# Kernel optimization log

Hardware: AMD Instinct MI355X
Metric: run time of the kernel (lower is better)

## Reference

```python
import jax, jax.numpy as jnp
import numpy as np

RADIUS, HEAD, SLOT, DIM = 16.0, 8, 112, 512

def _l2norm(x, axis):
    n = jnp.linalg.norm(x, axis=axis, keepdims=True)
    return x / jnp.maximum(n, 1e-12)

def _layernorm(x, g, b, eps=1e-5):
    mu = jnp.mean(x, axis=-1, keepdims=True)
    var = jnp.mean((x - mu) ** 2, axis=-1, keepdims=True)
    return (x - mu) / jnp.sqrt(var + eps) * g + b

def setup_inputs() -> dict:
    key = jax.random.key(0)
    ks = jax.random.split(key, 12)
    B, S = 32, 512
    return {
        "query": jax.random.normal(ks[0], (B, S, DIM), jnp.float32),
        "value": jax.random.normal(ks[1], (B, S, DIM), jnp.float32),
        "key_mem": jax.random.normal(ks[2], (HEAD * SLOT, DIM // HEAD), jnp.float32) * 0.5,
        "value_mem": jax.random.normal(ks[3], (SLOT, DIM), jnp.float32) * 0.5,
        "Wq": jax.random.normal(ks[4], (DIM, DIM), jnp.float32) * 0.02,
        "bq": jnp.zeros((DIM,), jnp.float32),
        "Wv": jax.random.normal(ks[5], (DIM, DIM), jnp.float32) * 0.02,
        "bv": jnp.zeros((DIM,), jnp.float32),
        "Wl": jax.random.normal(ks[6], (DIM, DIM * HEAD), jnp.float32) * 0.02,
        "bl": jnp.zeros((DIM,), jnp.float32),
        "g1": jnp.ones((DIM,), jnp.float32), "b1": jnp.zeros((DIM,), jnp.float32),
        "g2": jnp.ones((DIM,), jnp.float32), "b2": jnp.zeros((DIM,), jnp.float32),
        "g3": jnp.ones((DIM,), jnp.float32), "b3": jnp.zeros((DIM,), jnp.float32),
    }

def reference(query, value, key_mem, value_mem, Wq, bq, Wv, bv, Wl, bl,
              g1, b1, g2, b2, g3, b3):
    B, S, C = query.shape
    mq = query.reshape(B * S, C)                                   # (BS, 512)
    # --- key addressing (read path) ---
    key_norm = _l2norm(key_mem.reshape(HEAD, SLOT, -1), axis=2)    # (h, s, 64)
    eq = _l2norm((mq @ Wq.T + bq).reshape(B * S, HEAD, -1), axis=2)
    key_sim = jnp.einsum('bhd,hsd->bhs', eq, key_norm)             # (BS, h, s)
    key_add = jax.nn.softmax(RADIUS * key_sim, axis=2)
    m_head = jnp.einsum('bhs,sd->bhd', key_add,
                        jax.lax.stop_gradient(value_mem))          # (BS, h, 512)
    vir = _layernorm(m_head.reshape(B * S, HEAD * DIM) @ Wl.T + bl, g2, b2)
    te_fusion = _layernorm(query + vir.reshape(B, S, DIM), g1, b1)  # dropout = eval identity
    # --- value addressing (write/train path) ---
    mv = value.reshape(B * S, DIM)
    ev = jax.lax.stop_gradient(mv) @ Wv.T + bv
    value_norm = _l2norm(value_mem, axis=1)                        # (s, 512)
    value_sim = _l2norm(ev, axis=1) @ value_norm.T                 # (BS, s)
    value_add = jax.nn.softmax(RADIUS * value_sim, axis=1)
    aud = value_add @ value_mem                                    # (BS, 512)
    contrastive = 0.5 * jnp.abs(jnp.eye(SLOT, dtype=value_norm.dtype)
                                - value_norm @ value_norm.T).sum()[None]
    mvd = jax.lax.stop_gradient(mv)
    cos = (aud * mvd).sum(1) / jnp.maximum(
        jnp.linalg.norm(aud, axis=1) * jnp.linalg.norm(mvd, axis=1), 1e-8)
    recon = jnp.abs(1.0 - cos).reshape(B, S).sum(1)                # (B,)
    aud = _layernorm(aud, g3, b3)
    tr_fusion = _layernorm(query + aud.reshape(B, S, DIM), g1, b1)
    return (te_fusion, tr_fusion, recon, contrastive)
```

## Files before the change

### kernel.cpp

```cpp
#include <hip/hip_runtime.h>
#include <math.h>

#define DIMC   512
#define HEADS  8
#define SLOTS  112
#define HD     64
#define NROWS  16384
#define RADIUSF 16.0f

typedef short short8 __attribute__((ext_vector_type(8)));
typedef unsigned short ushort8 __attribute__((ext_vector_type(8)));
typedef float f32x4  __attribute__((ext_vector_type(4)));

__device__ __forceinline__ unsigned short f2bf(float f)
{
    unsigned u = __float_as_uint(f);
    unsigned r = (u + 0x7FFFu + ((u >> 16) & 1u)) >> 16;
    return (unsigned short)r;
}
__device__ __forceinline__ float bf2f(unsigned short h)
{
    return __uint_as_float((unsigned)h << 16);
}

__device__ __forceinline__ void gl16(const void* g, void* lds_wave_base)
{
    __builtin_amdgcn_global_load_lds(
        (const __attribute__((address_space(1))) unsigned int*)g,
        (__attribute__((address_space(3))) unsigned int*)lds_wave_base,
        16, 0, 0);
}

#define DPP_ADD(x, ctrl, rmask)                                               \
    (x) += __int_as_float(__builtin_amdgcn_update_dpp(                        \
               0, __float_as_int(x), (ctrl), (rmask), 0xf, true))

__device__ __forceinline__ float wsum64(float x)
{
    DPP_ADD(x, 0x111, 0xf);
    DPP_ADD(x, 0x112, 0xf);
    DPP_ADD(x, 0x114, 0xf);
    DPP_ADD(x, 0x118, 0xf);
    DPP_ADD(x, 0x142, 0xa);
    DPP_ADD(x, 0x143, 0xc);
    return __int_as_float(__builtin_amdgcn_readlane(__float_as_int(x), 63));
}

__device__ __forceinline__ void wsum64_4(float& a, float& b, float& c, float& d)
{
    DPP_ADD(a, 0x111, 0xf); DPP_ADD(b, 0x111, 0xf); DPP_ADD(c, 0x111, 0xf); DPP_ADD(d, 0x111, 0xf);
    DPP_ADD(a, 0x112, 0xf); DPP_ADD(b, 0x112, 0xf); DPP_ADD(c, 0x112, 0xf); DPP_ADD(d, 0x112, 0xf);
    DPP_ADD(a, 0x114, 0xf); DPP_ADD(b, 0x114, 0xf); DPP_ADD(c, 0x114, 0xf); DPP_ADD(d, 0x114, 0xf);
    DPP_ADD(a, 0x118, 0xf); DPP_ADD(b, 0x118, 0xf); DPP_ADD(c, 0x118, 0xf); DPP_ADD(d, 0x118, 0xf);
    DPP_ADD(a, 0x142, 0xa); DPP_ADD(b, 0x142, 0xa); DPP_ADD(c, 0x142, 0xa); DPP_ADD(d, 0x142, 0xa);
    DPP_ADD(a, 0x143, 0xc); DPP_ADD(b, 0x143, 0xc); DPP_ADD(c, 0x143, 0xc); DPP_ADD(d, 0x143, 0xc);
    a = __int_as_float(__builtin_amdgcn_readlane(__float_as_int(a), 63));
    b = __int_as_float(__builtin_amdgcn_readlane(__float_as_int(b), 63));
    c = __int_as_float(__builtin_amdgcn_readlane(__float_as_int(c), 63));
    d = __int_as_float(__builtin_amdgcn_readlane(__float_as_int(d), 63));
}

__global__ __launch_bounds__(256)
void gemm_bf16(const short* __restrict__ A, int lda,
               const short* __restrict__ B, int ldb,
               float* __restrict__ C, unsigned short* __restrict__ Cb,
               int ldc, int K, const float* __restrict__ bias, int Nvalid,
               int aZ, int bZ, int cZ)
{
    __shared__ short As[128 * 32];
    __shared__ short Bs[128 * 32];
    A += (size_t)blockIdx.z * aZ;
    B += (size_t)blockIdx.z * bZ;
    const size_t czoff = (size_t)blockIdx.z * cZ;
    const int tid  = threadIdx.x;
    const int wave = tid >> 6;
    const int lane = tid & 63;
    const int m0 = blockIdx.y * 128;
    const int n0 = blockIdx.x * 128;
    const int wm = (wave >> 1) * 64;
    const int wn = (wave & 1) * 64;

    const int srow = tid >> 2;
    const int schk = (tid & 3) * 8;

    const int fr = lane & 15;
    const int fq = (lane >> 4) * 8;

    f32x4 acc[4][4] = {};

    const short* Ag = A + (size_t)(m0 + srow) * lda + schk;
    const short* Bg = B + (size_t)(n0 + srow) * ldb + schk;

    short* asL = As + wave * 512;
    short* asU = As + 2048 + wave * 512;
    short* bsL = Bs + wave * 512;
    short* bsU = Bs + 2048 + wave * 512;

    for (int k0 = 0; k0 < K; k0 += 32) {
        gl16(Ag, asL);
        gl16(Ag + (size_t)64 * lda, asU);
        gl16(Bg, bsL);
        gl16(Bg + (size_t)64 * ldb, bsU);
        Ag += 32; Bg += 32;
        __syncthreads();
        short8 af[4], bf[4];
        #pragma unroll
        for (int i = 0; i < 4; ++i)
            af[i] = *(const short8*)&As[(wm + i * 16 + fr) * 32 + fq];
        #pragma unroll
        for (int j = 0; j < 4; ++j)
            bf[j] = *(const short8*)&Bs[(wn + j * 16 + fr) * 32 + fq];
        #pragma unroll
        for (int i = 0; i < 4; ++i)
            #pragma unroll
            for (int j = 0; j < 4; ++j)
                acc[i][j] = __builtin_amdgcn_mfma_f32_16x16x32_bf16(
                    af[i], bf[j], acc[i][j], 0, 0, 0);
        __syncthreads();
    }

    const int cr = (lane >> 4) * 4;
    const int cc = lane & 15;
    #pragma unroll
    for (int i = 0; i < 4; ++i) {
        const int grow = m0 + wm + i * 16 + cr;
        #pragma unroll
        for (int j = 0; j < 4; ++j) {
            const int gcol = n0 + wn + j * 16 + cc;
            if (gcol < Nvalid) {
                const float bb = bias ? bias[gcol] : 0.f;
                const size_t base = czoff + (size_t)grow * ldc + gcol;
                #pragma unroll
                for (int r = 0; r < 4; ++r) {
                    const float val = acc[i][j][r] + bb;
                    if (C)  C[base + (size_t)r * ldc]  = val;
                    if (Cb) Cb[base + (size_t)r * ldc] = f2bf(val);
                }
            }
        }
    }
}

__global__ __launch_bounds__(256)
void gemm_softmax(const short* __restrict__ A, int lda, int aZ,
                  const short* __restrict__ B, int ldb, int bZ,
                  int K,
                  unsigned short* __restrict__ Ob, int ldo, int oPerZ, int padN)
{
    __shared__ short As[128 * 32];
    __shared__ short Bs[128 * 32];
    __shared__ float P[128][113];
    __shared__ float hinvS[128];
    A += (size_t)blockIdx.z * aZ;
    B += (size_t)blockIdx.z * bZ;
    const int tid  = threadIdx.x;
    const int wave = tid >> 6;
    const int lane = tid & 63;
    const int m0 = blockIdx.y * 128;
    const int wm = (wave >> 1) * 64;
    const int wn = (wave & 1) * 64;
    const int srow = tid >> 2;
    const int schk = (tid & 3) * 8;
    const int fr = lane & 15;
    const int fq = (lane >> 4) * 8;

    f32x4 acc[4][4] = {};
    float ss[4] = {0.f, 0.f, 0.f, 0.f};

    const short* Ag = A + (size_t)(m0 + srow) * lda + schk;
    const short* Bg = B + (size_t)srow * ldb + schk;

    short* asL = As + wave * 512;
    short* asU = As + 2048 + wave * 512;
    short* bsL = Bs + wave * 512;
    short* bsU = Bs + 2048 + wave * 512;

    for (int k0 = 0; k0 < K; k0 += 32) {
        gl16(Ag, asL);
        gl16(Ag + (size_t)64 * lda, asU);
        gl16(Bg, bsL);
        gl16(Bg + (size_t)64 * ldb, bsU);
        Ag += 32; Bg += 32;
        __syncthreads();
        short8 af[4], bf[4];
        #pragma unroll
        for (int i = 0; i < 4; ++i)
            af[i] = *(const short8*)&As[(wm + i * 16 + fr) * 32 + fq];
        #pragma unroll
        for (int j = 0; j < 4; ++j)
            bf[j] = *(const short8*)&Bs[(wn + j * 16 + fr) * 32 + fq];
        #pragma unroll
        for (int i = 0; i < 4; ++i)
            #pragma unroll
            for (int e = 0; e < 8; ++e) {
                const float f = bf2f((unsigned short)af[i][e]);
                ss[i] += f * f;
            }
        #pragma unroll
        for (int i = 0; i < 4; ++i)
            #pragma unroll
            for (int j = 0; j < 4; ++j)
                acc[i][j] = __builtin_amdgcn_mfma_f32_16x16x32_bf16(
                    af[i], bf[j], acc[i][j], 0, 0, 0);
        __syncthreads();
    }

    #pragma unroll
    for (int i = 0; i < 4; ++i) {
        ss[i] += __shfl_xor(ss[i], 16, 64);
        ss[i] += __shfl_xor(ss[i], 32, 64);
    }
    if (lane < 16) {
        #pragma unroll
        for (int i = 0; i < 4; ++i)
            hinvS[wm + i * 16 + lane] = 1.f / fmaxf(sqrtf(ss[i]), 1e-12f);
    }

    const int cr = (lane >> 4) * 4;
    const int cc = lane & 15;
    #pragma unroll
    for (int i = 0; i < 4; ++i) {
        const int prow = wm + i * 16 + cr;
        #pragma unroll
        for (int j = 0; j < 4; ++j) {
            const int pcol = wn + j * 16 + cc;
            if (pcol < SLOTS) {
                #pragma unroll
                for (int r = 0; r < 4; ++r)
                    P[prow + r][pcol] = acc[i][j][r];
            }
        }
    }
    __syncthreads();

    const int rowt = tid >> 1;
    const int half = tid & 1;
    const int k0 = half * 56;
    const int rr = m0 + rowt;
    const float s = RADIUSF * hinvS[rowt];
    float mx = -1e30f;
    for (int k = k0; k < k0 + 56; ++k) mx = fmaxf(mx, P[rowt][k]);
    mx = fmaxf(mx, __shfl_xor(mx, 1, 64));
    float sum = 0.f;
    for (int k = k0; k < k0 + 56; ++k) {
        const float e = __expf(s * (P[rowt][k] - mx));
        P[rowt][k] = e;
        sum += e;
    }
    sum += __shfl_xor(sum, 1, 64);
    const float inv = 1.f / sum;
    unsigned short* orow = Ob + (size_t)rr * ldo + (size_t)blockIdx.z * oPerZ;
    for (int k = k0; k < k0 + 56; ++k) orow[k] = f2bf(P[rowt][k] * inv);
    if (half == 1)
        for (int k = SLOTS; k < padN; ++k) orow[k] = 0;
}

#define FUSED_LDS_DECL                                                        \
    __shared__ float U[17408];    \
    float* P = U;                                                             \
    short* As0 = (short*)U;                             \
    short* As1 = As0 + 1024;                            \
    short* Bs0 = As1 + 1024;                           \
    short* Bs1 = Bs0 + 16384;

#define FUSED_GEMM_CORE(Aptr, lda, Bptr, ldb, K)                              \
    f32x4 acc[2][4] = {};                                                     \
    {                                                                         \
        const int lrow = lane >> 2;                                           \
        const int lchk = (lane & 3) * 8;                                      \
        for (int k0 = 0; k0 < (K); k0 += 64) {                                \
            if (wave < 2)                                                     \
                gl16((Aptr) + (size_t)(m0 + wave * 16 + lrow) * (lda) + k0 + lchk, \
                     As0 + wave * 512);                                       \
            else if (wave < 4)                                                \
                gl16((Aptr) + (size_t)(m0 + (wave - 2) * 16 + lrow) * (lda) + k0 + 32 + lchk, \
                     As1 + (wave - 2) * 512);                                 \
            _Pragma("unroll")                                                 \
            for (int s = 0; s < 4; ++s) {                                     \
                const size_t brow = (size_t)(wave * 64 + s * 16 + lrow);      \
                gl16((Bptr) + brow * (ldb) + k0 + lchk,                       \
                     Bs0 + (wave * 64 + s * 16) * 32);                        \
                gl16((Bptr) + brow * (ldb) + k0 + 32 + lchk,                  \
                     Bs1 + (wave * 64 + s * 16) * 32);                        \
            }                                                                 \
            __syncthreads();                                                  \
            short8 af0[2], af1[2], bf0[4], bf1[4];                            \
            _Pragma("unroll")                                                 \
            for (int i = 0; i < 2; ++i) {                                     \
                af0[i] = *(const short8*)&As0[(i * 16 + fr) * 32 + fq];       \
                af1[i] = *(const short8*)&As1[(i * 16 + fr) * 32 + fq];       \
            }                                                                 \
            _Pragma("unroll")                                                 \
            for (int c = 0; c < 4; ++c) {                                     \
                bf0[c] = *(const short8*)&Bs0[(wave * 64 + c * 16 + fr) * 32 + fq]; \
                bf1[c] = *(const short8*)&Bs1[(wave * 64 + c * 16 + fr) * 32 + fq]; \
            }                                                                 \
            _Pragma("unroll")                                                 \
            for (int i = 0; i < 2; ++i)                                       \
                _Pragma("unroll")                                             \
                for (int c = 0; c < 4; ++c) {                                 \
                    acc[i][c] = __builtin_amdgcn_mfma_f32_16x16x32_bf16(      \
                        af0[i], bf0[c], acc[i][c], 0, 0, 0);                  \
                    acc[i][c] = __builtin_amdgcn_mfma_f32_16x16x32_bf16(      \
                        af1[i], bf1[c], acc[i][c], 0, 0, 0);                  \
                }                                                             \
            __syncthreads();                                                  \
        }                                                                     \
    }                                                                         \
    {                                                                         \
        const int cr = (lane >> 4) * 4;                                       \
        const int cc = lane & 15;                                             \
        _Pragma("unroll")                                                     \
        for (int i = 0; i < 2; ++i)                                           \
            _Pragma("unroll")                                                 \
            for (int c = 0; c < 4; ++c) {                                     \
                const int col = wave * 64 + c * 16 + cc;                      \
                _Pragma("unroll")                                             \
                for (int r = 0; r < 4; ++r)                                   \
                    P[(i * 16 + cr + r) * 516 + col] = acc[i][c][r];          \
            }                                                                 \
    }                                                                         \
    __syncthreads();

__global__ __launch_bounds__(512, 4)
void gemm_vir_te(const short* __restrict__ A, int lda,
                 const short* __restrict__ B, int ldb, int K,
                 const float* __restrict__ bias, const float* __restrict__ query,
                 const float* __restrict__ g1, const float* __restrict__ b1,
                 const float* __restrict__ g2, const float* __restrict__ b2,
                 float* __restrict__ out_te)
{
    FUSED_LDS_DECL
    const int tid = threadIdx.x;
    const int wave = tid >> 6;
    const int lane = tid & 63;
    const int m0 = blockIdx.x * 32;
    const int fr = lane & 15;
    const int fq = (lane >> 4) * 8;

    FUSED_GEMM_CORE(A, lda, B, ldb, K)

    const int c0 = lane * 8;
    float blv[8], gg2[8], bb2[8], gg1[8], bb1[8];
    *(f32x4*)&blv[0] = *(const f32x4*)(bias + c0);
    *(f32x4*)&blv[4] = *(const f32x4*)(bias + c0 + 4);
    *(f32x4*)&gg2[0] = *(const f32x4*)(g2 + c0);
    *(f32x4*)&gg2[4] = *(const f32x4*)(g2 + c0 + 4);
    *(f32x4*)&bb2[0] = *(const f32x4*)(b2 + c0);
    *(f32x4*)&bb2[4] = *(const f32x4*)(b2 + c0 + 4);
    *(f32x4*)&gg1[0] = *(const f32x4*)(g1 + c0);
    *(f32x4*)&gg1[4] = *(const f32x4*)(g1 + c0 + 4);
    *(f32x4*)&bb1[0] = *(const f32x4*)(b1 + c0);
    *(f32x4*)&bb1[4] = *(const f32x4*)(b1 + c0 + 4);

    for (int rp = 0; rp < 2; ++rp) {
        const int lr0 = wave * 4 + rp * 2;
        float x[2][8], q[2][8];
        #pragma unroll
        for (int p = 0; p < 2; ++p) {
            *(f32x4*)&x[p][0] = *(const f32x4*)&P[(lr0 + p) * 516 + c0];
            *(f32x4*)&x[p][4] = *(const f32x4*)&P[(lr0 + p) * 516 + c0 + 4];
            const size_t gbase = (size_t)(m0 + lr0 + p) * DIMC + c0;
            *(f32x4*)&q[p][0] = *(const f32x4*)(query + gbase);
            *(f32x4*)&q[p][4] = *(const f32x4*)(query + gbase + 4);
            #pragma unroll
            for (int j = 0; j < 8; ++j) x[p][j] += blv[j];
        }
        float s1[2] = {0.f, 0.f}, s2[2] = {0.f, 0.f};
        #pragma unroll
        for (int p = 0; p < 2; ++p)
            #pragma unroll
            for (int j = 0; j < 8; ++j) {
                s1[p] += x[p][j];
                s2[p] += x[p][j] * x[p][j];
            }
        wsum64_4(s1[0], s2[0], s1[1], s2[1]);

        float y[2][8];
        float t1[2] = {0.f, 0.f}, t2[2] = {0.f, 0.f};
        #pragma unroll
        for (int p = 0; p < 2; ++p) {
            const float mu = s1[p] * (1.f / DIMC);
            const float var = s2[p] * (1.f / DIMC) - mu * mu;
            const float rstd = rsqrtf(var + 1e-5f);
            #pragma unroll
            for (int j = 0; j < 8; ++j) {
                const float v = (x[p][j] - mu) * rstd * gg2[j] + bb2[j];
                y[p][j] = q[p][j] + v;
                t1[p] += y[p][j];
                t2[p] += y[p][j] * y[p][j];
            }
        }
        wsum64_4(t1[0], t2[0], t1[1], t2[1]);

        #pragma unroll
        for (int p = 0; p < 2; ++p) {
            const float mu = t1[p] * (1.f / DIMC);
            const float var = t2[p] * (1.f / DIMC) - mu * mu;
            const float rstd = rsqrtf(var + 1e-5f);
            float o[8];
            #pragma unroll
            for (int j = 0; j < 8; ++j)
                o[j] = (y[p][j] - mu) * rstd * gg1[j] + bb1[j];
            const size_t gbase = (size_t)(m0 + lr0 + p) * DIMC + c0;
            *(float4*)(out_te + gbase)     = make_float4(o[0], o[1], o[2], o[3]);
            *(float4*)(out_te + gbase + 4) = make_float4(o[4], o[5], o[6], o[7]);
        }
    }
}

__global__ __launch_bounds__(512, 4)
void gemm_aud_tr(const short* __restrict__ A, int lda,
                 const short* __restrict__ B, int ldb, int K,
                 const float* __restrict__ value, const float* __restrict__ query,
                 const float* __restrict__ g1, const float* __restrict__ b1,
                 const float* __restrict__ g3, const float* __restrict__ b3,
                 float* __restrict__ out_tr, float* __restrict__ recon)
{
    FUSED_LDS_DECL
    __shared__ float red[8];
    const int tid = threadIdx.x;
    const int wave = tid >> 6;
    const int lane = tid & 63;
    const int m0 = blockIdx.x * 32;
    const int fr = lane & 15;
    const int fq = (lane >> 4) * 8;

    FUSED_GEMM_CORE(A, lda, B, ldb, K)

    const int c0 = lane * 8;
    float gg3[8], bb3[8], gg1[8], bb1[8];
    *(f32x4*)&gg3[0] = *(const f32x4*)(g3 + c0);
    *(f32x4*)&gg3[4] = *(const f32x4*)(g3 + c0 + 4);
    *(f32x4*)&bb3[0] = *(const f32x4*)(b3 + c0);
    *(f32x4*)&bb3[4] = *(const f32x4*)(b3 + c0 + 4);
    *(f32x4*)&gg1[0] = *(const f32x4*)(g1 + c0);
    *(f32x4*)&gg1[4] = *(const f32x4*)(g1 + c0 + 4);
    *(f32x4*)&bb1[0] = *(const f32x4*)(b1 + c0);
    *(f32x4*)&bb1[4] = *(const f32x4*)(b1 + c0 + 4);

    float rloc = 0.f;
    for (int rp = 0; rp < 2; ++rp) {
        const int lr0 = wave * 4 + rp * 2;
        float a[2][8], v[2][8], q[2][8];
        #pragma unroll
        for (int p = 0; p < 2; ++p) {
            *(f32x4*)&a[p][0] = *(const f32x4*)&P[(lr0 + p) * 516 + c0];
            *(f32x4*)&a[p][4] = *(const f32x4*)&P[(lr0 + p) * 516 + c0 + 4];
            const size_t gbase = (size_t)(m0 + lr0 + p) * DIMC + c0;
            *(f32x4*)&v[p][0] = *(const f32x4*)(value + gbase);
            *(f32x4*)&v[p][4] = *(const f32x4*)(value + gbase + 4);
            *(f32x4*)&q[p][0] = *(const f32x4*)(query + gbase);
            *(f32x4*)&q[p][4] = *(const f32x4*)(query + gbase + 4);
        }
        float dot[2] = {0.f, 0.f}, na[2] = {0.f, 0.f};
        float nv[2] = {0.f, 0.f}, s1[2] = {0.f, 0.f};
        #pragma unroll
        for (int p = 0; p < 2; ++p)
            #pragma unroll
            for (int j = 0; j < 8; ++j) {
                dot[p] += a[p][j] * v[p][j];
                na[p]  += a[p][j] * a[p][j];
                nv[p]  += v[p][j] * v[p][j];
                s1[p]  += a[p][j];
            }
        wsum64_4(dot[0], na[0], nv[0], s1[0]);
        wsum64_4(dot[1], na[1], nv[1], s1[1]);

        #pragma unroll
        for (int p = 0; p < 2; ++p) {
            const float cosv = dot[p] / fmaxf(sqrtf(na[p]) * sqrtf(nv[p]), 1e-8f);
            rloc += fabsf(1.f - cosv);
        }

        float y[2][8];
        float t1[2] = {0.f, 0.f}, t2[2] = {0.f, 0.f};
        #pragma unroll
        for (int p = 0; p < 2; ++p) {
            const float mu = s1[p] * (1.f / DIMC);
            const float var = na[p] * (1.f / DIMC) - mu * mu;
            const float rstd = rsqrtf(var + 1e-5f);
            #pragma unroll
            for (int j = 0; j < 8; ++j) {
                const float w = (a[p][j] - mu) * rstd * gg3[j] + bb3[j];
                y[p][j] = q[p][j] + w;
                t1[p] += y[p][j];
                t2[p] += y[p][j] * y[p][j];
            }
        }
        wsum64_4(t1[0], t2[0], t1[1], t2[1]);

        #pragma unroll
        for (int p = 0; p < 2; ++p) {
            const float mu = t1[p] * (1.f / DIMC);
            const float var = t2[p] * (1.f / DIMC) - mu * mu;
            const float rstd = rsqrtf(var + 1e-5f);
            float o[8];
            #pragma unroll
            for (int j = 0; j < 8; ++j)
                o[j] = (y[p][j] - mu) * rstd * gg1[j] + bb1[j];
            const size_t gbase = (size_t)(m0 + lr0 + p) * DIMC + c0;
            *(float4*)(out_tr + gbase)     = make_float4(o[0], o[1], o[2], o[3]);
            *(float4*)(out_tr + gbase + 4) = make_float4(o[4], o[5], o[6], o[7]);
        }
    }

    if (lane == 0) red[wave] = rloc;
    __syncthreads();
    if (tid == 0)
        atomicAdd(&recon[m0 >> 9], red[0] + red[1] + red[2] + red[3]
                                 + red[4] + red[5] + red[6] + red[7]);
}

__device__ __forceinline__ float block_sum_256(float v, float* red)
{
    #pragma unroll
    for (int off = 32; off; off >>= 1) v += __shfl_down(v, off, 64);
    const int lane = threadIdx.x & 63, wid = threadIdx.x >> 6;
    __syncthreads();
    if (lane == 0) red[wid] = v;
    __syncthreads();
    return red[0] + red[1] + red[2] + red[3];
}

__global__ void conv_all(const float* __restrict__ q, const float* __restrict__ v,
                         const float* __restrict__ Wq, const float* __restrict__ Wv,
                         const float* __restrict__ Wl, const float* __restrict__ vm,
                         unsigned short* __restrict__ qbf, unsigned short* __restrict__ vbf,
                         unsigned short* __restrict__ wqbf, unsigned short* __restrict__ wvbf,
                         unsigned short* __restrict__ wlbf, unsigned short* __restrict__ vmbf)
{
    const int i = blockIdx.x * blockDim.x + threadIdx.x;
    const float* src;
    unsigned short* dst;
    int off;
    if (i < 2097152)      { src = q;  dst = qbf;  off = i; }
    else if (i < 4194304) { src = v;  dst = vbf;  off = i - 2097152; }
    else if (i < 4259840) { src = Wq; dst = wqbf; off = i - 4194304; }
    else if (i < 4325376) { src = Wv; dst = wvbf; off = i - 4259840; }
    else if (i < 4849664) { src = Wl; dst = wlbf; off = i - 4325376; }
    else if (i < 4864000) { src = vm; dst = vmbf; off = i - 4849664; }
    else {
        const int j = i - 4864000;
        *(ushort4*)(vmbf + 57344 + (size_t)j * 4) = make_ushort4(0, 0, 0, 0);
        return;
    }
    const float4 x = *(const float4*)(src + (size_t)off * 4);
    ushort4 o;
    o.x = f2bf(x.x); o.y = f2bf(x.y); o.z = f2bf(x.z); o.w = f2bf(x.w);
    *(ushort4*)(dst + (size_t)off * 4) = o;
}

__global__ void prep_key_norm(const float* __restrict__ km,
                              unsigned short* __restrict__ knb,
                              float* __restrict__ outrc)
{
    const int row = blockIdx.x;
    const int h = row >> 7, s = row & 127;
    const int lane = threadIdx.x;
    if (row == 0 && lane < 33) outrc[lane] = 0.f;
    const float v = (s < SLOTS) ? km[(size_t)(h * SLOTS + s) * HD + lane] : 0.f;
    const float ssum = wsum64(v * v);
    const float inv = 1.f / fmaxf(sqrtf(ssum), 1e-12f);
    knb[(size_t)row * HD + lane] = f2bf(v * inv);
}

__global__ void prep_value_norm(const float* __restrict__ vm,
                                float* __restrict__ vn,
                                unsigned short* __restrict__ vnb,
                                unsigned short* __restrict__ vmTb)
{
    const int row = blockIdx.x;
    const int tid = threadIdx.x;
    if (row >= 112) {
        const int idx = (row - 112) * 256 + tid;
        if (idx < 8192) {
            vmTb[(size_t)(idx >> 4) * 128 + 112 + (idx & 15)] = 0;
        } else {
            const int j = idx - 8192;
            vnb[(size_t)(112 + (j >> 9)) * 512 + (j & 511)] = 0;
        }
        return;
    }
    __shared__ float red[4];
    const float v0 = vm[(size_t)row * DIMC + tid];
    const float v1 = vm[(size_t)row * DIMC + 256 + tid];
    const float tot = block_sum_256(v0 * v0 + v1 * v1, red);
    const float inv = 1.f / fmaxf(sqrtf(tot), 1e-12f);
    vn[(size_t)row * DIMC + tid]        = v0 * inv;
    vn[(size_t)row * DIMC + 256 + tid]  = v1 * inv;
    vnb[(size_t)row * DIMC + tid]       = f2bf(v0 * inv);
    vnb[(size_t)row * DIMC + 256 + tid] = f2bf(v1 * inv);
    vmTb[(size_t)tid * 128 + row]         = f2bf(v0);
    vmTb[(size_t)(256 + tid) * 128 + row] = f2bf(v1);
}

__global__ void contrastive_kernel(const float* __restrict__ vn, float* __restrict__ outc)
{
    __shared__ float vni[DIMC];
    __shared__ float red[2];
    const int i = blockIdx.x, tid = threadIdx.x;
    for (int d = tid; d < DIMC; d += 128) vni[d] = vn[(size_t)i * DIMC + d];
    __syncthreads();
    float t = 0.f;
    if (tid < SLOTS) {
        const float* r = vn + (size_t)tid * DIMC;
        float dot = 0.f;
        for (int d = 0; d < DIMC; ++d) dot += vni[d] * r[d];
        const float delta = (tid == i) ? 1.f : 0.f;
        t = fabsf(delta - dot);
    }
    #pragma unroll
    for (int off = 32; off; off >>= 1) t += __shfl_down(t, off, 64);
    if ((tid & 63) == 0) red[tid >> 6] = t;
    __syncthreads();
    if (tid == 0) atomicAdd(outc, 0.5f * (red[0] + red[1]));
}

extern "C" void kernel_launch(void* const* d_in, const int* in_sizes, int n_in,
                              void* d_out, int out_size, void* d_ws, size_t ws_size,
                              hipStream_t stream)
{
    const float* query = (const float*)d_in[0];
    const float* value = (const float*)d_in[1];
    const float* keym  = (const float*)d_in[2];
    const float* vmem  = (const float*)d_in[3];
    const float* Wq    = (const float*)d_in[4];
    const float* bq    = (const float*)d_in[5];
    const float* Wv    = (const float*)d_in[6];
    const float* bv    = (const float*)d_in[7];
    const float* Wl    = (const float*)d_in[8];
    const float* bl    = (const float*)d_in[9];
    const float* g1    = (const float*)d_in[10];
    const float* b1    = (const float*)d_in[11];
    const float* g2    = (const float*)d_in[12];
    const float* b2    = (const float*)d_in[13];
    const float* g3    = (const float*)d_in[14];
    const float* b3    = (const float*)d_in[15];

    float* out    = (float*)d_out;
    float* out_te = out;
    float* out_tr = out + 8388608;
    float* out_rc = out + 16777216;

    float* ws = (float*)d_ws;
    unsigned short* w_knb  = (unsigned short*)(ws + 0);
    unsigned short* w_vmTb = (unsigned short*)(ws + 32768);
    unsigned short* w_vnb  = (unsigned short*)(ws + 65536);
    float*          w_vn   = ws + 98304;
    unsigned short* w_w2tbf= (unsigned short*)(ws + 155648);
    unsigned short* w_vmbf = (unsigned short*)(ws + 385024);
    unsigned short* w_wlbf = (unsigned short*)(ws + 417792);
    unsigned short* w_xbf  = (unsigned short*)(ws + 1466368);
    unsigned short* w_kaddc= (unsigned short*)(ws + 5660672);
    unsigned short* w_vsb  = (unsigned short*)(ws + 13000704);
    unsigned short* w_qbf  = (unsigned short*)(ws + 14049280);
    unsigned short* w_vbf  = (unsigned short*)(ws + 18243584);
    unsigned short* w_wqbf = (unsigned short*)(ws + 22437888);
    unsigned short* w_wvbf = (unsigned short*)(ws + 22568960);

    conv_all<<<19008, 256, 0, stream>>>(query, value, Wq, Wv, Wl, vmem,
                                        w_qbf, w_vbf, w_wqbf, w_wvbf,
                                        w_wlbf, w_vmbf);
    prep_key_norm<<<1024, 64, 0, stream>>>(keym, w_knb, out_rc);
    prep_value_norm<<<176, 256, 0, stream>>>(vmem, w_vn, w_vnb, w_vmTb);
    contrastive_kernel<<<112, 128, 0, stream>>>(w_vn, out_rc + 32);
    gemm_bf16<<<dim3(1, 4, 8), 256, 0, stream>>>(
        (const short*)w_wlbf, HEADS * DIMC, (const short*)w_vmbf, DIMC,
        nullptr, w_w2tbf, HEADS * SLOTS, DIMC, nullptr, SLOTS,
        DIMC, 0, SLOTS);

    gemm_bf16<<<dim3(4, 128), 256, 0, stream>>>(
        (const short*)w_qbf, DIMC, (const short*)w_wqbf, DIMC,
        nullptr, w_xbf, DIMC, DIMC, bq, DIMC, 0, 0, 0);
    gemm_softmax<<<dim3(1, 128, 8), 256, 0, stream>>>(
        (const short*)w_xbf, DIMC, HD, (const short*)w_knb, HD, 128 * HD,
        HD, w_kaddc, HEADS * SLOTS, SLOTS, SLOTS);
    gemm_vir_te<<<NROWS / 32, 512, 0, stream>>>(
        (const short*)w_kaddc, HEADS * SLOTS, (const short*)w_w2tbf, HEADS * SLOTS,
        HEADS * SLOTS, bl, query, g1, b1, g2, b2, out_te);

    gemm_bf16<<<dim3(4, 128), 256, 0, stream>>>(
        (const short*)w_vbf, DIMC, (const short*)w_wvbf, DIMC,
        nullptr, w_xbf, DIMC, DIMC, bv, DIMC, 0, 0, 0);
    gemm_softmax<<<dim3(1, 128, 1), 256, 0, stream>>>(
        (const short*)w_xbf, DIMC, 0, (const short*)w_vnb, DIMC, 0,
        DIMC, w_vsb, 128, 0, 128);
    gemm_aud_tr<<<NROWS / 32, 512, 0, stream>>>(
        (const short*)w_vsb, 128, (const short*)w_vmTb, 128, 128,
        value, query, g1, b1, g3, b3, out_tr, out_rc);
}
```

Before: 329.4 us.

## Retile vir GEMM to 64-row blocks with register-resident double layernorm epilogue

Rewrites the vir/te fused GEMM so each block computes 64 rows instead of 32. Each of the 8 waves owns a 16x256 tile, so every B tile loaded into shared memory is reused across twice as many rows. The layernorm epilogue now runs directly on the MFMA accumulators using shuffle and shared-memory row reductions, skipping the staging of the output tile through LDS. The costs are higher register and LDS use (launch bounds drop to 2 blocks per CU), half as many blocks, and uncoalesced scalar loads of query and stores of out_te in the epilogue.

```diff
diff --git a/kernel.cpp b/kernel.cpp
--- a/kernel.cpp
+++ b/kernel.cpp
@@ -253,6 +253,166 @@
     for (int k = k0; k < k0 + 56; ++k) orow[k] = f2bf(P[rowt][k] * inv);
     if (half == 1)
         for (int k = SLOTS; k < padN; ++k) orow[k] = 0;
+}
+
+__global__ __launch_bounds__(512, 2)
+void gemm_vir_te(const short* __restrict__ A, int lda,
+                 const short* __restrict__ B, int ldb, int K,
+                 const float* __restrict__ bias, const float* __restrict__ query,
+                 const float* __restrict__ g1, const float* __restrict__ b1,
+                 const float* __restrict__ g2, const float* __restrict__ b2,
+                 float* __restrict__ out_te)
+{
+    __shared__ short As0[64 * 32];
+    __shared__ short As1[64 * 32];
+    __shared__ short Bs0[512 * 32];
+    __shared__ short Bs1[512 * 32];
+    __shared__ float parm[5 * 512];
+    __shared__ float red1[128], red2[128];
+
+    const int tid  = threadIdx.x;
+    const int wave = tid >> 6;
+    const int lane = tid & 63;
+    const int m0 = blockIdx.x * 64;
+    const int s = wave >> 1;
+    const int h = wave & 1;
+    const int fr = lane & 15;
+    const int fq = (lane >> 4) * 8;
+
+    parm[tid]        = bias[tid];
+    parm[512 + tid]  = g2[tid];
+    parm[1024 + tid] = b2[tid];
+    parm[1536 + tid] = g1[tid];
+    parm[2048 + tid] = b1[tid];
+
+    f32x4 acc[16] = {};
+
+    const int lrow = lane >> 2;
+    const int lchk = (lane & 3) * 8;
+
+    for (int k0 = 0; k0 < K; k0 += 64) {
+        if (wave < 4)
+            gl16(A + (size_t)(m0 + wave * 16 + lrow) * lda + k0 + lchk,
+                 As0 + wave * 512);
+        else
+            gl16(A + (size_t)(m0 + (wave - 4) * 16 + lrow) * lda + k0 + 32 + lchk,
+                 As1 + (wave - 4) * 512);
+        #pragma unroll
+        for (int s4 = 0; s4 < 4; ++s4) {
+            const size_t br = (size_t)(wave * 64 + s4 * 16 + lrow);
+            gl16(B + br * ldb + k0 + lchk,      Bs0 + (wave * 64 + s4 * 16) * 32);
+            gl16(B + br * ldb + k0 + 32 + lchk, Bs1 + (wave * 64 + s4 * 16) * 32);
+        }
+        __syncthreads();
+        const short8 af0 = *(const short8*)&As0[(s * 16 + fr) * 32 + fq];
+        const short8 af1 = *(const short8*)&As1[(s * 16 + fr) * 32 + fq];
+        #pragma unroll
+        for (int c = 0; c < 16; ++c) {
+            const short8 bf0 = *(const short8*)&Bs0[(h * 256 + c * 16 + fr) * 32 + fq];
+            acc[c] = __builtin_amdgcn_mfma_f32_16x16x32_bf16(af0, bf0, acc[c], 0, 0, 0);
+            const short8 bf1 = *(const short8*)&Bs1[(h * 256 + c * 16 + fr) * 32 + fq];
+            acc[c] = __builtin_amdgcn_mfma_f32_16x16x32_bf16(af1, bf1, acc[c], 0, 0, 0);
+        }
+        __syncthreads();
+    }
+
+    const int cc = lane & 15;
+    const int cr = (lane >> 4) * 4;
+    const int rowb = s * 16 + cr;
+
+    float s1[4] = {0.f, 0.f, 0.f, 0.f}, s2[4] = {0.f, 0.f, 0.f, 0.f};
+    #pragma unroll
+    for (int c = 0; c < 16; ++c) {
+        const float blc = parm[h * 256 + c * 16 + cc];
+        #pragma unroll
+        for (int r = 0; r < 4; ++r) {
+            const float x = acc[c][r] + blc;
+            s1[r] += x;
+            s2[r] += x * x;
+        }
+    }
+    #pragma unroll
+    for (int k = 1; k < 16; k <<= 1)
+        #pragma unroll
+        for (int r = 0; r < 4; ++r) {
+            s1[r] += __shfl_xor(s1[r], k, 16);
+            s2[r] += __shfl_xor(s2[r], k, 16);
+        }
+    if (cc == 0)
+        #pragma unroll
+        for (int r = 0; r < 4; ++r) {
+            red1[(rowb + r) * 2 + h] = s1[r];
+            red2[(rowb + r) * 2 + h] = s2[r];
+        }
+    __syncthreads();
+    float mu[4], rs[4];
+    #pragma unroll
+    for (int r = 0; r < 4; ++r) {
+        const float t1 = red1[(rowb + r) * 2] + red1[(rowb + r) * 2 + 1];
+        const float t2 = red2[(rowb + r) * 2] + red2[(rowb + r) * 2 + 1];
+        mu[r] = t1 * (1.f / DIMC);
+        const float var = t2 * (1.f / DIMC) - mu[r] * mu[r];
+        rs[r] = rsqrtf(var + 1e-5f);
+    }
+    __syncthreads();
+
+    float t1[4] = {0.f, 0.f, 0.f, 0.f}, t2[4] = {0.f, 0.f, 0.f, 0.f};
+    #pragma unroll
+    for (int c = 0; c < 16; ++c) {
+        const int col = h * 256 + c * 16 + cc;
+        const float blc = parm[col];
+        const float g2c = parm[512 + col];
+        const float b2c = parm[1024 + col];
+        #pragma unroll
+        for (int r = 0; r < 4; ++r) {
+            const float x = acc[c][r] + blc;
+            const float qv = query[(size_t)(m0 + rowb + r) * DIMC + col];
+            const float y = qv + (x - mu[r]) * rs[r] * g2c + b2c;
+            t1[r] += y;
+            t2[r] += y * y;
+        }
+    }
+    #pragma unroll
+    for (int k = 1; k < 16; k <<= 1)
+        #pragma unroll
+        for (int r = 0; r < 4; ++r) {
+            t1[r] += __shfl_xor(t1[r], k, 16);
+            t2[r] += __shfl_xor(t2[r], k, 16);
+        }
+    if (cc == 0)
+        #pragma unroll
+        for (int r = 0; r < 4; ++r) {
+            red1[(rowb + r) * 2 + h] = t1[r];
+            red2[(rowb + r) * 2 + h] = t2[r];
+        }
+    __syncthreads();
+    float mu2[4], rs2[4];
+    #pragma unroll
+    for (int r = 0; r < 4; ++r) {
+        const float u1 = red1[(rowb + r) * 2] + red1[(rowb + r) * 2 + 1];
+        const float u2 = red2[(rowb + r) * 2] + red2[(rowb + r) * 2 + 1];
+        mu2[r] = u1 * (1.f / DIMC);
+        const float var = u2 * (1.f / DIMC) - mu2[r] * mu2[r];
+        rs2[r] = rsqrtf(var + 1e-5f);
+    }
+
+    #pragma unroll
+    for (int c = 0; c < 16; ++c) {
+        const int col = h * 256 + c * 16 + cc;
+        const float blc = parm[col];
+        const float g2c = parm[512 + col];
+        const float b2c = parm[1024 + col];
+        const float g1c = parm[1536 + col];
+        const float b1c = parm[2048 + col];
+        #pragma unroll
+        for (int r = 0; r < 4; ++r) {
+            const float x = acc[c][r] + blc;
+            const float qv = query[(size_t)(m0 + rowb + r) * DIMC + col];
+            const float y = qv + (x - mu[r]) * rs[r] * g2c + b2c;
+            out_te[(size_t)(m0 + rowb + r) * DIMC + col] =
+                (y - mu2[r]) * rs2[r] * g1c + b1c;
+        }
+    }
 }
 
 #define FUSED_LDS_DECL                                                        \
@@ -323,93 +483,6 @@
     __syncthreads();
 
 __global__ __launch_bounds__(512, 4)
-void gemm_vir_te(const short* __restrict__ A, int lda,
-                 const short* __restrict__ B, int ldb, int K,
-                 const float* __restrict__ bias, const float* __restrict__ query,
-                 const float* __restrict__ g1, const float* __restrict__ b1,
-                 const float* __restrict__ g2, const float* __restrict__ b2,
-                 float* __restrict__ out_te)
-{
-    FUSED_LDS_DECL
-    const int tid = threadIdx.x;
-    const int wave = tid >> 6;
-    const int lane = tid & 63;
-    const int m0 = blockIdx.x * 32;
-    const int fr = lane & 15;
-    const int fq = (lane >> 4) * 8;
-
-    FUSED_GEMM_CORE(A, lda, B, ldb, K)
-
-    const int c0 = lane * 8;
-    float blv[8], gg2[8], bb2[8], gg1[8], bb1[8];
-    *(f32x4*)&blv[0] = *(const f32x4*)(bias + c0);
-    *(f32x4*)&blv[4] = *(const f32x4*)(bias + c0 + 4);
-    *(f32x4*)&gg2[0] = *(const f32x4*)(g2 + c0);
-    *(f32x4*)&gg2[4] = *(const f32x4*)(g2 + c0 + 4);
-    *(f32x4*)&bb2[0] = *(const f32x4*)(b2 + c0);
-    *(f32x4*)&bb2[4] = *(const f32x4*)(b2 + c0 + 4);
-    *(f32x4*)&gg1[0] = *(const f32x4*)(g1 + c0);
-    *(f32x4*)&gg1[4] = *(const f32x4*)(g1 + c0 + 4);
-    *(f32x4*)&bb1[0] = *(const f32x4*)(b1 + c0);
-    *(f32x4*)&bb1[4] = *(const f32x4*)(b1 + c0 + 4);
-
-    for (int rp = 0; rp < 2; ++rp) {
-        const int lr0 = wave * 4 + rp * 2;
-        float x[2][8], q[2][8];
-        #pragma unroll
-        for (int p = 0; p < 2; ++p) {
-            *(f32x4*)&x[p][0] = *(const f32x4*)&P[(lr0 + p) * 516 + c0];
-            *(f32x4*)&x[p][4] = *(const f32x4*)&P[(lr0 + p) * 516 + c0 + 4];
-            const size_t gbase = (size_t)(m0 + lr0 + p) * DIMC + c0;
-            *(f32x4*)&q[p][0] = *(const f32x4*)(query + gbase);
-            *(f32x4*)&q[p][4] = *(const f32x4*)(query + gbase + 4);
-            #pragma unroll
-            for (int j = 0; j < 8; ++j) x[p][j] += blv[j];
-        }
-        float s1[2] = {0.f, 0.f}, s2[2] = {0.f, 0.f};
-        #pragma unroll
-        for (int p = 0; p < 2; ++p)
-            #pragma unroll
-            for (int j = 0; j < 8; ++j) {
-                s1[p] += x[p][j];
-                s2[p] += x[p][j] * x[p][j];
-            }
-        wsum64_4(s1[0], s2[0], s1[1], s2[1]);
-
-        float y[2][8];
-        float t1[2] = {0.f, 0.f}, t2[2] = {0.f, 0.f};
-        #pragma unroll
-        for (int p = 0; p < 2; ++p) {
-            const float mu = s1[p] * (1.f / DIMC);
-            const float var = s2[p] * (1.f / DIMC) - mu * mu;
-            const float rstd = rsqrtf(var + 1e-5f);
-            #pragma unroll
-            for (int j = 0; j < 8; ++j) {
-                const float v = (x[p][j] - mu) * rstd * gg2[j] + bb2[j];
-                y[p][j] = q[p][j] + v;
-                t1[p] += y[p][j];
-                t2[p] += y[p][j] * y[p][j];
-            }
-        }
-        wsum64_4(t1[0], t2[0], t1[1], t2[1]);
-
-        #pragma unroll
-        for (int p = 0; p < 2; ++p) {
-            const float mu = t1[p] * (1.f / DIMC);
-            const float var = t2[p] * (1.f / DIMC) - mu * mu;
-            const float rstd = rsqrtf(var + 1e-5f);
-            float o[8];
-            #pragma unroll
-            for (int j = 0; j < 8; ++j)
-                o[j] = (y[p][j] - mu) * rstd * gg1[j] + bb1[j];
-            const size_t gbase = (size_t)(m0 + lr0 + p) * DIMC + c0;
-            *(float4*)(out_te + gbase)     = make_float4(o[0], o[1], o[2], o[3]);
-            *(float4*)(out_te + gbase + 4) = make_float4(o[4], o[5], o[6], o[7]);
-        }
-    }
-}
-
-__global__ __launch_bounds__(512, 4)
 void gemm_aud_tr(const short* __restrict__ A, int lda,
                  const short* __restrict__ B, int ldb, int K,
                  const float* __restrict__ value, const float* __restrict__ query,
@@ -676,7 +749,7 @@
     gemm_softmax<<<dim3(1, 128, 8), 256, 0, stream>>>(
         (const short*)w_xbf, DIMC, HD, (const short*)w_knb, HD, 128 * HD,
         HD, w_kaddc, HEADS * SLOTS, SLOTS, SLOTS);
-    gemm_vir_te<<<NROWS / 32, 512, 0, stream>>>(
+    gemm_vir_te<<<NROWS / 64, 512, 0, stream>>>(
         (const short*)w_kaddc, HEADS * SLOTS, (const short*)w_w2tbf, HEADS * SLOTS,
         HEADS * SLOTS, bl, query, g1, b1, g2, b2, out_te);
 
```

New measurement: 341.2 us. 1.04x slower.
